# Kernel optimization log

Measured on AMD Instinct MI355X. Metric: run time of the kernel, lower is better.

## Reference

```python
import jax, jax.numpy as jnp
import numpy as np

# CUBA-LIF constants (from LavaNetwork.__init__ with beta=0.95)
THRESHOLD = 1.0
CURRENT_DECAY = 1.0   # current[t] = (1-1.0)*current[t-1] + input[t] == input[t]
VOLTAGE_DECAY = 1.0 - 0.95  # = 0.05, so v[t] = 0.95*v[t-1] + cur[t]

N_INPUT, N_HIDDEN, N_OUTPUT = 512, 2048, 4 * 64
B, T = 32, 1024


def setup_inputs() -> dict:
    key = jax.random.key(0)
    kx, k1, k2, k3, k4 = jax.random.split(key, 5)
    x = (jax.random.uniform(kx, (B, N_INPUT, T)) < 0.1).astype(jnp.float32)
    # learned params (Linear with bias); small scale so spiking is reasonable
    w1 = jax.random.normal(k1, (N_HIDDEN, N_INPUT), dtype=jnp.float32) * (1.0 / np.sqrt(N_INPUT))
    b1 = jax.random.normal(k2, (N_HIDDEN,), dtype=jnp.float32) * 0.01
    w2 = jax.random.normal(k3, (N_OUTPUT, N_HIDDEN), dtype=jnp.float32) * (1.0 / np.sqrt(N_HIDDEN))
    b2 = jax.random.normal(k4, (N_OUTPUT,), dtype=jnp.float32) * 0.01
    return {"x": x, "w1": w1, "b1": b1, "w2": w2, "b2": b2}


def _cuba_lif(cur):
    """CUBA neuron with current_decay=1 (current==synaptic input),
    leaky-integrate voltage, fire at threshold, reset voltage to 0.
    cur: (B, N, T) -> spikes (B, N, T)."""
    beta_v = 1.0 - VOLTAGE_DECAY  # 0.95

    def step(v, c_t):
        v = v * beta_v + c_t
        s = (v >= THRESHOLD).astype(v.dtype)
        v = v * (1.0 - s)  # reset-to-zero on spike (Loihi behavior)
        return v, s

    cur_t = jnp.moveaxis(cur, -1, 0)  # (T, B, N)
    v0 = jnp.zeros(cur.shape[:-1], cur.dtype)
    _, spk = jax.lax.scan(step, v0, cur_t)
    return jnp.moveaxis(spk, 0, -1)  # (B, N, T)


def reference(x, w1, b1, w2, b2):
    # layer 1: synapse (einsum 'bit,oi->bot' + bias) -> CUBA neuron
    cur1 = jnp.einsum('bit,oi->bot', x, w1) + b1[None, :, None]
    spk1 = _cuba_lif(cur1)
    # layer 2
    cur2 = jnp.einsum('bit,oi->bot', spk1, w2) + b2[None, :, None]
    spk2 = _cuba_lif(cur2)
    return (spk1, spk2)
```

## Files before the change

kernel.cpp:

```cpp
#include <hip/hip_runtime.h>


typedef int i32x4 __attribute__((ext_vector_type(4)));
typedef _Float16 f16x8 __attribute__((ext_vector_type(8)));
typedef _Float16 f16x4 __attribute__((ext_vector_type(4)));
typedef float f32x4 __attribute__((ext_vector_type(4)));

#define GLDS(g, l) __builtin_amdgcn_global_load_lds( \
    (const __attribute__((address_space(1))) void*)(g), \
    (__attribute__((address_space(3))) void*)(l), 16, 0, 0)

#define INV231 4.656612873077392578125e-10


__global__ __launch_bounds__(256) void prep_w8(const float* __restrict__ A,
                                               signed char* __restrict__ wp,
                                               int M, int K)
{
    long gt = (long)blockIdx.x * 256 + threadIdx.x;
    int kq4 = K >> 2;
    int m = (int)(gt / kq4), kq = (int)(gt % kq4);
    int k0 = kq * 4;
    int kt = k0 >> 6, kin = k0 & 63;
    int cw = ((kin >> 4) ^ (m >> 1)) & 3;
    float4 w = *(const float4*)&A[(long)m * K + k0];
    float wv[4] = {w.x, w.y, w.z, w.w};
    int pack[4] = {0, 0, 0, 0};
#pragma unroll
    for (int e = 0; e < 4; e++) {
        long k64 = (long)rint((double)wv[e] * 2147483648.0);
#pragma unroll
        for (int j = 0; j < 3; j++) {
            long r = ((k64 + 128) & 255) - 128;
            pack[j] |= ((int)r & 255) << (e * 8);
            k64 = (k64 - r) >> 8;
        }
        pack[3] |= ((int)k64 & 255) << (e * 8);
    }
#pragma unroll
    for (int p = 0; p < 4; p++)
        *(int*)&wp[(((long)kt * 4 + p) * M + m) * 64 + cw * 16 + (kin & 15)] = pack[p];
}

__global__ __launch_bounds__(256) void prep_x8(const float* __restrict__ x,
                                               unsigned char* __restrict__ xt)
{
    __shared__ float xs[64][68];
    const int b = blockIdx.z, i0 = blockIdx.y * 64, t0 = blockIdx.x * 64;
    const float* xb = x + ((long)b * 512 + i0) * 1024 + t0;
#pragma unroll
    for (int p = 0; p < 4; p++) {
        int f = threadIdx.x + p * 256;
        int i = f >> 4, t4 = (f & 15) * 4;
        *(float4*)&xs[i][t4] = *(const float4*)&xb[(long)i * 1024 + t4];
    }
    __syncthreads();
    int tt = threadIdx.x >> 2, c = threadIdx.x & 3;
    unsigned char bytes[16];
#pragma unroll
    for (int j = 0; j < 16; j++)
        bytes[j] = (unsigned char)xs[c * 16 + j][tt];
    *(uint4*)&xt[(((long)b * 8 + (i0 >> 6)) * 1024 + t0 + tt) * 64 + c * 16] =
        *(uint4*)bytes;
}

__global__ __launch_bounds__(576, 1) void gemm_lif1(
    const signed char* __restrict__ wp,
    const unsigned char* __restrict__ act,
    const float* __restrict__ bias,
    unsigned* __restrict__ mask_ws)
{
    __shared__ signed char Ws[8][4][64][64];
    __shared__ float cs[2][64][64];

    const int m0 = blockIdx.x * 64, b = blockIdx.y;
    const int tid = threadIdx.x, lane = tid & 63, wave = tid >> 6;
    const int lm = lane & 15, lq = lane >> 4;
    const int fro = ((lq ^ (lm >> 1)) & 3) * 16;
    const int mw = wave & 3;
    const int tw2 = wave >> 2;
    const unsigned char* ab = act + (long)b * 8 * 1024 * 64;

    i32x4 areg[4][2];
    double bv = 0.0;

    if (wave < 8) {
        const int gl_row = lane >> 2, gl_col = (lane & 3) * 16;
#pragma unroll
        for (int j = 0; j < 4; ++j) {
            const int r = wave + 8 * j;
            const int kt = r >> 2, pl = r & 3;
            const signed char* g = wp + ((long)r * 2048 + m0 + gl_row) * 64 + gl_col;
#pragma unroll
            for (int q = 0; q < 4; ++q)
                GLDS(g + q * 16 * 64, &Ws[kt][pl][q * 16][0]);
        }
        bv = (double)bias[m0 + mw * 16 + lm];
#pragma unroll
        for (int f = 0; f < 2; f++)
            areg[0][f] = *(const i32x4*)
                &ab[((long)(tw2 * 32 + f * 16 + lm)) * 64 + lq * 16];
#pragma unroll
        for (int f = 0; f < 2; f++)
            areg[1][f] = *(const i32x4*)
                &ab[((long)1 * 1024 + tw2 * 32 + f * 16 + lm) * 64 + lq * 16];
    }
    __syncthreads();

    double u = 0.0;
    bool sprev = false;

    for (int p = 0; p < 17; ++p) {
        if (wave < 8 && p < 16) {
            i32x4 acc[4][2];
#pragma unroll
            for (int pp = 0; pp < 4; pp++)
#pragma unroll
                for (int f = 0; f < 2; f++) acc[pp][f] = (i32x4)0;

#pragma unroll
            for (int kk = 0; kk < 8; ++kk) {
                {
                    int vn = p * 8 + kk + 2;
                    if (vn > 127) vn = 127;
                    const int pn = vn >> 3, kn = vn & 7;
                    const long tt = (long)pn * 64 + tw2 * 32 + lm;
#pragma unroll
                    for (int f = 0; f < 2; f++)
                        areg[(kk + 2) & 3][f] = *(const i32x4*)
                            &ab[((long)kn * 1024 + tt + f * 16) * 64 + lq * 16];
                }
                __builtin_amdgcn_s_setprio(1);
#pragma unroll
                for (int pl = 0; pl < 4; pl++) {
                    i32x4 w0 = *(const i32x4*)&Ws[kk][pl][mw * 16 + lm][fro];
#pragma unroll
                    for (int f = 0; f < 2; f++)
                        acc[pl][f] = __builtin_amdgcn_mfma_i32_16x16x64_i8(
                            areg[kk & 3][f], w0, acc[pl][f], 0, 0, 0);
                }
                __builtin_amdgcn_s_setprio(0);
            }
#pragma unroll
            for (int tf = 0; tf < 2; tf++)
#pragma unroll
                for (int r = 0; r < 4; r++) {
                    long T = acc[3][tf][r];
                    T = T * 256 + acc[2][tf][r];
                    T = T * 256 + acc[1][tf][r];
                    T = T * 256 + acc[0][tf][r];
                    cs[p & 1][tw2 * 32 + tf * 16 + lq * 4 + r][mw * 16 + lm] =
                        (float)((double)T * INV231 + bv);
                }
        }
        if (wave == 8 && p >= 1) {
            const int pq = p - 1, buf = pq & 1;
            float cvA[32], cvB[32];
#pragma unroll
            for (int j = 0; j < 32; ++j) cvA[j] = cs[buf][j][lane];
#pragma unroll
            for (int j = 0; j < 32; ++j) cvB[j] = cs[buf][32 + j][lane];
            {
                unsigned mword = 0;
#pragma unroll
                for (int j = 0; j < 32; ++j) {
                    double c = (double)cvA[j];
                    double a = 0.95 * u + c;
                    u = sprev ? c : a;
                    bool s = (u >= 1.0);
                    mword |= (s ? 1u : 0u) << j;
                    sprev = s;
                }
                mask_ws[((long)b * 32 + pq * 2 + 0) * 2048 + m0 + lane] = mword;
            }
            {
                unsigned mword = 0;
#pragma unroll
                for (int j = 0; j < 32; ++j) {
                    double c = (double)cvB[j];
                    double a = 0.95 * u + c;
                    u = sprev ? c : a;
                    bool s = (u >= 1.0);
                    mword |= (s ? 1u : 0u) << j;
                    sprev = s;
                }
                mask_ws[((long)b * 32 + pq * 2 + 1) * 2048 + m0 + lane] = mword;
            }
        }
        asm volatile("s_waitcnt lgkmcnt(0)" ::: "memory");
        __builtin_amdgcn_s_barrier();
        __builtin_amdgcn_sched_barrier(0);
    }
}

__global__ __launch_bounds__(256) void expand_both(
    const unsigned* __restrict__ mask_ws,
    unsigned char* __restrict__ spk8,
    float* __restrict__ spk1)
{
    __shared__ unsigned msk[64][33];
    const int b = blockIdx.x, kt = blockIdx.y;
    const int tid = threadIdx.x;
#pragma unroll
    for (int i = 0; i < 8; ++i) {
        int idx = tid + i * 256;
        int tw = idx >> 6, m = idx & 63;
        msk[m][tw] = mask_ws[((long)b * 32 + tw) * 2048 + kt * 64 + m];
    }
    __syncthreads();
    unsigned char* dst = spk8 + ((long)b * 32 + kt) * 1024 * 64;
#pragma unroll
    for (int i = 0; i < 16; ++i) {
        int off = tid + i * 256;
        int t = off >> 2, mq = off & 3;
        int tw = t >> 5, sh = t & 31;
        unsigned w0 = 0, w1 = 0, w2 = 0, w3 = 0;
#pragma unroll
        for (int j = 0; j < 4; ++j) {
            w0 |= ((msk[mq * 16 + j][tw] >> sh) & 1u) << (8 * j);
            w1 |= ((msk[mq * 16 + 4 + j][tw] >> sh) & 1u) << (8 * j);
            w2 |= ((msk[mq * 16 + 8 + j][tw] >> sh) & 1u) << (8 * j);
            w3 |= ((msk[mq * 16 + 12 + j][tw] >> sh) & 1u) << (8 * j);
        }
        *(uint4*)&dst[(long)off * 16] = (uint4){w0, w1, w2, w3};
    }
    const int rr = tid >> 5, l5 = tid & 31;
    const int sh1 = (l5 & 7) * 4;
#pragma unroll
    for (int rep = 0; rep < 8; ++rep) {
        const int row = rr + rep * 8;
        float* d1 = spk1 + ((long)b * 2048 + kt * 64 + row) * 1024;
#pragma unroll
        for (int j = 0; j < 8; j++) {
            const int t = l5 * 4 + j * 128;
            const unsigned w = msk[row][(l5 >> 3) + j * 4];
            float4 o;
            o.x = ((w >> sh1) & 1u) ? 1.f : 0.f;
            o.y = ((w >> (sh1 + 1)) & 1u) ? 1.f : 0.f;
            o.z = ((w >> (sh1 + 2)) & 1u) ? 1.f : 0.f;
            o.w = ((w >> (sh1 + 3)) & 1u) ? 1.f : 0.f;
            *(float4*)&d1[t] = o;
        }
    }
}

__global__ __launch_bounds__(320, 1) void gemm_lif2(
    const signed char* __restrict__ wp,
    const unsigned char* __restrict__ act,
    const float* __restrict__ bias,
    float* __restrict__ spk2)
{
    __shared__ signed char Ws[32][4][16][64];
    __shared__ float cs[2][128][17];

    const int b = blockIdx.x, m0 = blockIdx.y * 16;
    const int tid = threadIdx.x, lane = tid & 63, wave = tid >> 6;
    const int lm = lane & 15, lq = lane >> 4;
    const int fro = ((lq ^ (lm >> 1)) & 3) * 16;
    const unsigned char* ab = act + (long)b * 32 * 1024 * 64;

    i32x4 areg[4][2];
    double bvr[4] = {0.0, 0.0, 0.0, 0.0};

    if (wave < 4) {
        const int gl_row = lane >> 2, gl_col = (lane & 3) * 16;
#pragma unroll
        for (int j = 0; j < 32; ++j) {
            const int r = wave + 4 * j;
            const int kt = r >> 2, pl = r & 3;
            const signed char* g =
                wp + (((long)kt * 4 + pl) * 256 + m0 + gl_row) * 64 + gl_col;
            GLDS(g, &Ws[kt][pl][0][0]);
        }
#pragma unroll
        for (int r = 0; r < 4; ++r)
            bvr[r] = (double)bias[m0 + lq * 4 + r];
        {
            const long wt0 = wave * 32 + lm;
#pragma unroll
            for (int f = 0; f < 2; f++)
                areg[0][f] = *(const i32x4*)&ab[(wt0 + f * 16) * 64 + lq * 16];
#pragma unroll
            for (int f = 0; f < 2; f++)
                areg[1][f] = *(const i32x4*)
                    &ab[((long)1 * 1024 + wt0 + f * 16) * 64 + lq * 16];
        }
    }
    __syncthreads();

    double u = 0.0;
    bool sprev = false;
    float* sp2 = spk2 + ((long)b * 256 + m0 + (lane & 15)) * 1024;

    for (int p = 0; p < 9; ++p) {
        if (wave < 4 && p < 8) {
            i32x4 acc[4][2];
#pragma unroll
            for (int pp = 0; pp < 4; pp++)
#pragma unroll
                for (int f = 0; f < 2; f++) acc[pp][f] = (i32x4)0;

#pragma unroll 4
            for (int kt = 0; kt < 32; ++kt) {
                {
                    int vn = p * 32 + kt + 2;
                    if (vn > 255) vn = 255;
                    const int pn = vn >> 5, kn = vn & 31;
                    const long tt = (long)pn * 128 + wave * 32 + lm;
#pragma unroll
                    for (int f = 0; f < 2; f++)
                        areg[(kt + 2) & 3][f] = *(const i32x4*)
                            &ab[((long)kn * 1024 + tt + f * 16) * 64 + lq * 16];
                }
                __builtin_amdgcn_s_setprio(1);
#pragma unroll
                for (int pl = 0; pl < 4; pl++) {
                    i32x4 w0 = *(const i32x4*)&Ws[kt][pl][lm][fro];
#pragma unroll
                    for (int f = 0; f < 2; f++)
                        acc[pl][f] = __builtin_amdgcn_mfma_i32_16x16x64_i8(
                            w0, areg[kt & 3][f], acc[pl][f], 0, 0, 0);
                }
                __builtin_amdgcn_s_setprio(0);
            }
#pragma unroll
            for (int tf = 0; tf < 2; tf++)
#pragma unroll
                for (int r = 0; r < 4; r++) {
                    long T = acc[3][tf][r];
                    T = T * 256 + acc[2][tf][r];
                    T = T * 256 + acc[1][tf][r];
                    T = T * 256 + acc[0][tf][r];
                    cs[p & 1][wave * 32 + tf * 16 + lm][lq * 4 + r] =
                        (float)((double)T * INV231 + bvr[r]);
                }
        }
        if (wave == 4 && p >= 1 && lane < 16) {
            const int pq = p - 1, buf = pq & 1;
            float* sp = sp2 + pq * 128;
            float cvA[32], cvB[32];
#pragma unroll
            for (int j = 0; j < 32; ++j) cvA[j] = cs[buf][j][lane];
#pragma unroll
            for (int j = 0; j < 32; ++j) cvB[j] = cs[buf][32 + j][lane];
            {
#pragma unroll
                for (int j = 0; j < 32; ++j) {
                    double c = (double)cvA[j];
                    double a = 0.95 * u + c;
                    u = sprev ? c : a;
                    bool s = (u >= 1.0);
                    sp[j] = s ? 1.f : 0.f;
                    sprev = s;
                }
            }
#pragma unroll
            for (int j = 0; j < 32; ++j) cvA[j] = cs[buf][64 + j][lane];
            {
#pragma unroll
                for (int j = 0; j < 32; ++j) {
                    double c = (double)cvB[j];
                    double a = 0.95 * u + c;
                    u = sprev ? c : a;
                    bool s = (u >= 1.0);
                    sp[32 + j] = s ? 1.f : 0.f;
                    sprev = s;
                }
            }
#pragma unroll
            for (int j = 0; j < 32; ++j) cvB[j] = cs[buf][96 + j][lane];
            {
#pragma unroll
                for (int j = 0; j < 32; ++j) {
                    double c = (double)cvA[j];
                    double a = 0.95 * u + c;
                    u = sprev ? c : a;
                    bool s = (u >= 1.0);
                    sp[64 + j] = s ? 1.f : 0.f;
                    sprev = s;
                }
            }
            {
#pragma unroll
                for (int j = 0; j < 32; ++j) {
                    double c = (double)cvB[j];
                    double a = 0.95 * u + c;
                    u = sprev ? c : a;
                    bool s = (u >= 1.0);
                    sp[96 + j] = s ? 1.f : 0.f;
                    sprev = s;
                }
            }
        }
        asm volatile("s_waitcnt lgkmcnt(0)" ::: "memory");
        __builtin_amdgcn_s_barrier();
        __builtin_amdgcn_sched_barrier(0);
    }
}


__device__ inline void split3(float w, _Float16& q0, _Float16& q1, _Float16& q2) {
    float p0 = rintf(w * 4096.f) * 2.44140625e-4f;
    float r1 = w - p0;
    float p1s = rintf(r1 * 8388608.f) * 2.44140625e-4f;
    float r2 = r1 - p1s * 4.8828125e-4f;
    float p2s = rintf(r2 * 1.7179869184e10f) * 1.220703125e-4f;
    q0 = (_Float16)p0; q1 = (_Float16)p1s; q2 = (_Float16)p2s;
}

__global__ __launch_bounds__(256) void gemm_f16x3_kernel(
    const float* __restrict__ A, const float* __restrict__ Bmat,
    const float* __restrict__ bias, float* __restrict__ C,
    int M, int N, int K, long sB, long sC)
{
    __shared__ _Float16 As[3][128][40];
    __shared__ _Float16 Bsh[128][40];
    const int batch = blockIdx.z;
    const float* Bp = Bmat + (long)batch * sB;
    float* Cp = C + (long)batch * sC;
    const int m0 = blockIdx.y * 128, n0 = blockIdx.x * 128;
    const int tid = threadIdx.x, lane = tid & 63, wave = tid >> 6;
    const int wrow = (wave >> 1) * 64, wcol = (wave & 1) * 64;
    const int lm = lane & 15, lq = lane >> 4;
    const int a_mo = tid >> 3, a_kc = (tid & 7) * 4;
    const int b_kq = tid >> 5, b_nq = tid & 31;

    f32x4 acc[3][4][4];
#pragma unroll
    for (int p = 0; p < 3; p++)
#pragma unroll
        for (int i = 0; i < 4; i++)
#pragma unroll
            for (int j = 0; j < 4; j++) acc[p][i][j] = (f32x4)0.f;

    for (int k0 = 0; k0 < K; k0 += 32) {
#pragma unroll
        for (int i = 0; i < 4; i++) {
            const int m = i * 32 + a_mo;
            float4 w = *(const float4*)&A[(long)(m0 + m) * K + k0 + a_kc];
            _Float16 a0[4], a1[4], a2[4];
            split3(w.x, a0[0], a1[0], a2[0]);
            split3(w.y, a0[1], a1[1], a2[1]);
            split3(w.z, a0[2], a1[2], a2[2]);
            split3(w.w, a0[3], a1[3], a2[3]);
            *(f16x4*)&As[0][m][a_kc] = (f16x4){a0[0], a0[1], a0[2], a0[3]};
            *(f16x4*)&As[1][m][a_kc] = (f16x4){a1[0], a1[1], a1[2], a1[3]};
            *(f16x4*)&As[2][m][a_kc] = (f16x4){a2[0], a2[1], a2[2], a2[3]};
        }
        {
            float4 r0 = *(const float4*)&Bp[(long)(k0 + b_kq * 4 + 0) * N + n0 + b_nq * 4];
            float4 r1 = *(const float4*)&Bp[(long)(k0 + b_kq * 4 + 1) * N + n0 + b_nq * 4];
            float4 r2 = *(const float4*)&Bp[(long)(k0 + b_kq * 4 + 2) * N + n0 + b_nq * 4];
            float4 r3 = *(const float4*)&Bp[(long)(k0 + b_kq * 4 + 3) * N + n0 + b_nq * 4];
            *(f16x4*)&Bsh[b_nq * 4 + 0][b_kq * 4] =
                (f16x4){(_Float16)r0.x, (_Float16)r1.x, (_Float16)r2.x, (_Float16)r3.x};
            *(f16x4*)&Bsh[b_nq * 4 + 1][b_kq * 4] =
                (f16x4){(_Float16)r0.y, (_Float16)r1.y, (_Float16)r2.y, (_Float16)r3.y};
            *(f16x4*)&Bsh[b_nq * 4 + 2][b_kq * 4] =
                (f16x4){(_Float16)r0.z, (_Float16)r1.z, (_Float16)r2.z, (_Float16)r3.z};
            *(f16x4*)&Bsh[b_nq * 4 + 3][b_kq * 4] =
                (f16x4){(_Float16)r0.w, (_Float16)r1.w, (_Float16)r2.w, (_Float16)r3.w};
        }
        __syncthreads();
        f16x8 bf[4];
#pragma unroll
        for (int j = 0; j < 4; j++)
            bf[j] = *(const f16x8*)&Bsh[wcol + j * 16 + lm][lq * 8];
#pragma unroll
        for (int p = 0; p < 3; p++) {
            f16x8 af[4];
#pragma unroll
            for (int i = 0; i < 4; i++)
                af[i] = *(const f16x8*)&As[p][wrow + i * 16 + lm][lq * 8];
#pragma unroll
            for (int i = 0; i < 4; i++)
#pragma unroll
                for (int j = 0; j < 4; j++)
                    acc[p][i][j] = __builtin_amdgcn_mfma_f32_16x16x32_f16(
                        af[i], bf[j], acc[p][i][j], 0, 0, 0);
        }
        __syncthreads();
    }
#pragma unroll
    for (int i = 0; i < 4; i++)
#pragma unroll
        for (int r = 0; r < 4; r++) {
            const int row = m0 + wrow + i * 16 + lq * 4 + r;
            const double bv = (double)bias[row];
#pragma unroll
            for (int j = 0; j < 4; j++) {
                double s = (double)acc[0][i][j][r]
                         + (double)acc[1][i][j][r] * 4.8828125e-4
                         + (double)acc[2][i][j][r] * 4.76837158203125e-7 + bv;
                Cp[(long)row * N + n0 + wcol + j * 16 + lm] = (float)s;
            }
        }
}

__global__ __launch_bounds__(256) void lif_rows(float* __restrict__ data,
                                                long nrows, int T)
{
    long r = (long)blockIdx.x * blockDim.x + threadIdx.x;
    if (r >= nrows) return;
    float* p = data + r * (long)T;
    double v = 0.0;
    for (int t = 0; t < T; t += 4) {
        float4 c = *(float4*)(p + t);
        float4 s;
        v = 0.95 * v + (double)c.x; s.x = (v >= 1.0) ? 1.f : 0.f; if (v >= 1.0) v = 0.0;
        v = 0.95 * v + (double)c.y; s.y = (v >= 1.0) ? 1.f : 0.f; if (v >= 1.0) v = 0.0;
        v = 0.95 * v + (double)c.z; s.z = (v >= 1.0) ? 1.f : 0.f; if (v >= 1.0) v = 0.0;
        v = 0.95 * v + (double)c.w; s.w = (v >= 1.0) ? 1.f : 0.f; if (v >= 1.0) v = 0.0;
        *(float4*)(p + t) = s;
    }
}


extern "C" void kernel_launch(void* const* d_in, const int* in_sizes, int n_in,
                              void* d_out, int out_size, void* d_ws, size_t ws_size,
                              hipStream_t stream)
{
    const float* x  = (const float*)d_in[0];
    const float* w1 = (const float*)d_in[1];
    const float* b1 = (const float*)d_in[2];
    const float* w2 = (const float*)d_in[3];
    const float* b2 = (const float*)d_in[4];

    float* out  = (float*)d_out;
    float* spk1 = out;
    float* spk2 = out + (long)32 * 2048 * 1024;

    const size_t WP1 = 4194304;
    const size_t WP2 = 2097152;
    const size_t X8T = 16777216;
    const size_t SPK = 67108864;
    const size_t MSK = 8388608;
    const size_t NEED = WP1 + WP2 + X8T + SPK + MSK;

    if (ws_size >= NEED) {
        char* ws = (char*)d_ws;
        signed char* wp1 = (signed char*)ws;
        signed char* wp2 = (signed char*)(ws + WP1);
        unsigned char* x8t = (unsigned char*)(ws + WP1 + WP2);
        unsigned char* spk8 = (unsigned char*)(ws + WP1 + WP2 + X8T);
        unsigned* mask_ws = (unsigned*)(ws + WP1 + WP2 + X8T + SPK);

        prep_w8<<<1024, 256, 0, stream>>>(w1, wp1, 2048, 512);
        prep_w8<<<512, 256, 0, stream>>>(w2, wp2, 256, 2048);
        prep_x8<<<dim3(16, 8, 32), 256, 0, stream>>>(x, x8t);

        gemm_lif1<<<dim3(32, 32), 576, 0, stream>>>(wp1, x8t, b1, mask_ws);

        expand_both<<<dim3(32, 32), 256, 0, stream>>>(mask_ws, spk8, spk1);

        gemm_lif2<<<dim3(32, 16), 320, 0, stream>>>(wp2, spk8, b2, spk2);
    } else {
        gemm_f16x3_kernel<<<dim3(8, 16, 32), 256, 0, stream>>>(
            w1, x, b1, spk1, 2048, 1024, 512, (long)512 * 1024, (long)2048 * 1024);
        lif_rows<<<(65536 + 255) / 256, 256, 0, stream>>>(spk1, 65536, 1024);
        gemm_f16x3_kernel<<<dim3(8, 2, 32), 256, 0, stream>>>(
            w2, spk1, b2, spk2, 256, 1024, 2048, (long)2048 * 1024, (long)256 * 1024);
        lif_rows<<<(8192 + 255) / 256, 256, 0, stream>>>(spk2, 8192, 1024);
    }
}
```

Before: 644.6 us.

## Split layer-2 GEMM across eight MMA waves and merge weight-prep launches

The layer-2 fused GEMM+LIF kernel now uses 8 compute waves, each covering 16 time columns, instead of 4 waves each covering 32. The LIF scan wave moves to wave index 8 and the block grows to 576 threads. Per-wave accumulators and activation registers shrink, which gives more latency hiding per block. The two weight-quantisation launches are also merged into one kernel to save a launch, at the cost of a larger block with the same single serial LIF consumer.

Measured after the change: 631.3 us, median of 2. 1.02x faster.

```diff
diff --git a/kernel.cpp b/kernel.cpp
--- a/kernel.cpp
+++ b/kernel.cpp
@@ -13,11 +13,11 @@
 #define INV231 4.656612873077392578125e-10
 
 
-__global__ __launch_bounds__(256) void prep_w8(const float* __restrict__ A,
-                                               signed char* __restrict__ wp,
-                                               int M, int K)
-{
-    long gt = (long)blockIdx.x * 256 + threadIdx.x;
+__device__ __forceinline__ void prep_w8_body(const float* __restrict__ A,
+                                             signed char* __restrict__ wp,
+                                             int M, int K, int bid, int tid)
+{
+    long gt = (long)bid * 256 + tid;
     int kq4 = K >> 2;
     int m = (int)(gt / kq4), kq = (int)(gt % kq4);
     int k0 = kq * 4;
@@ -40,6 +40,16 @@
 #pragma unroll
     for (int p = 0; p < 4; p++)
         *(int*)&wp[(((long)kt * 4 + p) * M + m) * 64 + cw * 16 + (kin & 15)] = pack[p];
+}
+
+__global__ __launch_bounds__(256) void prep_w8_both(
+    const float* __restrict__ w1, signed char* __restrict__ wp1,
+    const float* __restrict__ w2, signed char* __restrict__ wp2)
+{
+    if (blockIdx.x < 1024)
+        prep_w8_body(w1, wp1, 2048, 512, blockIdx.x, threadIdx.x);
+    else
+        prep_w8_body(w2, wp2, 256, 2048, blockIdx.x - 1024, threadIdx.x);
 }
 
 __global__ __launch_bounds__(256) void prep_x8(const float* __restrict__ x,
@@ -244,7 +254,7 @@
     }
 }
 
-__global__ __launch_bounds__(320, 1) void gemm_lif2(
+__global__ __launch_bounds__(576, 1) void gemm_lif2(
     const signed char* __restrict__ wp,
     const unsigned char* __restrict__ act,
     const float* __restrict__ bias,
@@ -259,14 +269,14 @@
     const int fro = ((lq ^ (lm >> 1)) & 3) * 16;
     const unsigned char* ab = act + (long)b * 32 * 1024 * 64;
 
-    i32x4 areg[4][2];
+    i32x4 areg[4];
     double bvr[4] = {0.0, 0.0, 0.0, 0.0};
 
-    if (wave < 4) {
+    if (wave < 8) {
         const int gl_row = lane >> 2, gl_col = (lane & 3) * 16;
 #pragma unroll
-        for (int j = 0; j < 32; ++j) {
-            const int r = wave + 4 * j;
+        for (int j = 0; j < 16; ++j) {
+            const int r = wave + 8 * j;
             const int kt = r >> 2, pl = r & 3;
             const signed char* g =
                 wp + (((long)kt * 4 + pl) * 256 + m0 + gl_row) * 64 + gl_col;
@@ -276,14 +286,9 @@
         for (int r = 0; r < 4; ++r)
             bvr[r] = (double)bias[m0 + lq * 4 + r];
         {
-            const long wt0 = wave * 32 + lm;
-#pragma unroll
-            for (int f = 0; f < 2; f++)
-                areg[0][f] = *(const i32x4*)&ab[(wt0 + f * 16) * 64 + lq * 16];
-#pragma unroll
-            for (int f = 0; f < 2; f++)
-                areg[1][f] = *(const i32x4*)
-                    &ab[((long)1 * 1024 + wt0 + f * 16) * 64 + lq * 16];
+            const long wt0 = wave * 16 + lm;
+            areg[0] = *(const i32x4*)&ab[wt0 * 64 + lq * 16];
+            areg[1] = *(const i32x4*)&ab[((long)1 * 1024 + wt0) * 64 + lq * 16];
         }
     }
     __syncthreads();
@@ -293,12 +298,10 @@
     float* sp2 = spk2 + ((long)b * 256 + m0 + (lane & 15)) * 1024;
 
     for (int p = 0; p < 9; ++p) {
-        if (wave < 4 && p < 8) {
-            i32x4 acc[4][2];
-#pragma unroll
-            for (int pp = 0; pp < 4; pp++)
-#pragma unroll
-                for (int f = 0; f < 2; f++) acc[pp][f] = (i32x4)0;
+        if (wave < 8 && p < 8) {
+            i32x4 acc[4];
+#pragma unroll
+            for (int pp = 0; pp < 4; pp++) acc[pp] = (i32x4)0;
 
 #pragma unroll 4
             for (int kt = 0; kt < 32; ++kt) {
@@ -306,36 +309,30 @@
                     int vn = p * 32 + kt + 2;
                     if (vn > 255) vn = 255;
                     const int pn = vn >> 5, kn = vn & 31;
-                    const long tt = (long)pn * 128 + wave * 32 + lm;
-#pragma unroll
-                    for (int f = 0; f < 2; f++)
-                        areg[(kt + 2) & 3][f] = *(const i32x4*)
-                            &ab[((long)kn * 1024 + tt + f * 16) * 64 + lq * 16];
+                    const long tt = (long)pn * 128 + wave * 16 + lm;
+                    areg[(kt + 2) & 3] = *(const i32x4*)
+                        &ab[((long)kn * 1024 + tt) * 64 + lq * 16];
                 }
                 __builtin_amdgcn_s_setprio(1);
 #pragma unroll
                 for (int pl = 0; pl < 4; pl++) {
                     i32x4 w0 = *(const i32x4*)&Ws[kt][pl][lm][fro];
-#pragma unroll
-                    for (int f = 0; f < 2; f++)
-                        acc[pl][f] = __builtin_amdgcn_mfma_i32_16x16x64_i8(
-                            w0, areg[kt & 3][f], acc[pl][f], 0, 0, 0);
+                    acc[pl] = __builtin_amdgcn_mfma_i32_16x16x64_i8(
+                        w0, areg[kt & 3], acc[pl], 0, 0, 0);
                 }
                 __builtin_amdgcn_s_setprio(0);
             }
 #pragma unroll
-            for (int tf = 0; tf < 2; tf++)
-#pragma unroll
-                for (int r = 0; r < 4; r++) {
-                    long T = acc[3][tf][r];
-                    T = T * 256 + acc[2][tf][r];
-                    T = T * 256 + acc[1][tf][r];
-                    T = T * 256 + acc[0][tf][r];
-                    cs[p & 1][wave * 32 + tf * 16 + lm][lq * 4 + r] =
-                        (float)((double)T * INV231 + bvr[r]);
-                }
-        }
-        if (wave == 4 && p >= 1 && lane < 16) {
+            for (int r = 0; r < 4; r++) {
+                long T = acc[3][r];
+                T = T * 256 + acc[2][r];
+                T = T * 256 + acc[1][r];
+                T = T * 256 + acc[0][r];
+                cs[p & 1][wave * 16 + lm][lq * 4 + r] =
+                    (float)((double)T * INV231 + bvr[r]);
+            }
+        }
+        if (wave == 8 && p >= 1 && lane < 16) {
             const int pq = p - 1, buf = pq & 1;
             float* sp = sp2 + pq * 128;
             float cvA[32], cvB[32];
@@ -545,15 +542,14 @@
         unsigned char* spk8 = (unsigned char*)(ws + WP1 + WP2 + X8T);
         unsigned* mask_ws = (unsigned*)(ws + WP1 + WP2 + X8T + SPK);
 
-        prep_w8<<<1024, 256, 0, stream>>>(w1, wp1, 2048, 512);
-        prep_w8<<<512, 256, 0, stream>>>(w2, wp2, 256, 2048);
+        prep_w8_both<<<1536, 256, 0, stream>>>(w1, wp1, w2, wp2);
         prep_x8<<<dim3(16, 8, 32), 256, 0, stream>>>(x, x8t);
 
         gemm_lif1<<<dim3(32, 32), 576, 0, stream>>>(wp1, x8t, b1, mask_ws);
 
         expand_both<<<dim3(32, 32), 256, 0, stream>>>(mask_ws, spk8, spk1);
 
-        gemm_lif2<<<dim3(32, 16), 320, 0, stream>>>(wp2, spk8, b2, spk2);
+        gemm_lif2<<<dim3(32, 16), 576, 0, stream>>>(wp2, spk8, b2, spk2);
     } else {
         gemm_f16x3_kernel<<<dim3(8, 16, 32), 256, 0, stream>>>(
             w1, x, b1, spk1, 2048, 1024, 512, (long)512 * 1024, (long)2048 * 1024);
```
